# Kernel tuning notes

Measured on AMD Instinct MI355X. Metric: run time of the kernel, lower is better.

The kernel has to match this reference:

```python
import jax, jax.numpy as jnp
import numpy as np

EPS = 1e-5
NH_MHA = 8
NH_GCN = 4


def _ln(x, w, b):
    m = x.mean(-1, keepdims=True)
    v = ((x - m) ** 2).mean(-1, keepdims=True)
    return (x - m) * jax.lax.rsqrt(v + EPS) * w + b


def _mha(t, in_w, in_b, out_w, out_b):
    # torch nn.MultiheadAttention (batch_first, eval mode -> no dropout)
    B, N, C = t.shape
    hd = C // NH_MHA
    qkv = t @ in_w.T + in_b
    q, k, v = jnp.split(qkv, 3, axis=-1)
    q = q.reshape(B, N, NH_MHA, hd)
    k = k.reshape(B, N, NH_MHA, hd)
    v = v.reshape(B, N, NH_MHA, hd)
    s = jnp.einsum('bihd,bjhd->bhij', q, k) * (1.0 / np.sqrt(hd))
    a = jax.nn.softmax(s, axis=-1)
    o = jnp.einsum('bhij,bjhd->bihd', a, v).reshape(B, N, C)
    return o @ out_w.T + out_b


def _gcn(x, v_w, v_b, e1_w, e1_b, eln_w, eln_b, e2_w, e2_b, o_w, o_b, n_w, n_b):
    # GraphConvolutionNetwork.forward (query/key branches are computed but
    # unused in the original -> omitted, identical math)
    B, N, C = x.shape
    hd = C // NH_GCN
    # edge MLP: split first linear so the [B,N,N,2C] concat is never built
    w1a, w1b = e1_w[:, :C], e1_w[:, C:]
    e = (x @ w1a.T)[:, :, None, :] + (x @ w1b.T)[:, None, :, :] + e1_b  # [B,N,N,C]
    e = jax.nn.gelu(_ln(e, eln_w, eln_b), approximate=False)
    ew = e @ e2_w.T + e2_b                 # [B,Ni,Nj,H]
    adj = jax.nn.softmax(ew, axis=2)       # softmax over Nj (== dim=-1 after permute in torch)
    v = (x @ v_w.T + v_b).reshape(B, N, NH_GCN, hd)
    out = jnp.einsum('bijh,bjhd->bihd', adj, v).reshape(B, N, C)
    out = out @ o_w.T + o_b
    return _ln(out + x, n_w, n_b)          # in_features == out_features -> residual


def reference(x, mha_in_w, mha_in_b, mha_out_w, mha_out_b,
              g0_v_w, g0_v_b, g0_e1_w, g0_e1_b, g0_eln_w, g0_eln_b, g0_e2_w, g0_e2_b, g0_o_w, g0_o_b, g0_n_w, g0_n_b,
              g1_v_w, g1_v_b, g1_e1_w, g1_e1_b, g1_eln_w, g1_eln_b, g1_e2_w, g1_e2_b, g1_o_w, g1_o_b, g1_n_w, g1_n_b,
              n1_w, n1_b, n2_w, n2_b,
              f1_w, f1_b, fln_w, fln_b, f2_w, f2_b):
    B, C, H, W = x.shape
    tokens = x.reshape(B, C, H * W).transpose(0, 2, 1)  # b c h w -> b (h w) c
    attn = _mha(tokens, mha_in_w, mha_in_b, mha_out_w, mha_out_b)
    attn = _ln(attn + tokens, n1_w, n1_b)
    g = _gcn(attn, g0_v_w, g0_v_b, g0_e1_w, g0_e1_b, g0_eln_w, g0_eln_b, g0_e2_w, g0_e2_b, g0_o_w, g0_o_b, g0_n_w, g0_n_b)
    g = _gcn(g, g1_v_w, g1_v_b, g1_e1_w, g1_e1_b, g1_eln_w, g1_eln_b, g1_e2_w, g1_e2_b, g1_o_w, g1_o_b, g1_n_w, g1_n_b)
    g = _ln(g, n2_w, n2_b)
    cat = jnp.concatenate([attn, g], axis=-1)           # [B,N,2C]
    f = cat @ f1_w.T + f1_b
    f = jax.nn.gelu(_ln(f, fln_w, fln_b), approximate=False)
    f = f @ f2_w.T + f2_b
    out = tokens + f
    return out.transpose(0, 2, 1).reshape(B, C, H, W)


def setup_inputs() -> dict:
    key = jax.random.key(0)
    ks = jax.random.split(key, 8)
    B, C, H, W = 2, 128, 24, 24
    f32 = jnp.float32

    def w(k, shape):
        return jax.random.normal(k, shape, f32) * 0.02

    d = {"x": jax.random.normal(ks[0], (B, C, H, W), f32)}
    d["mha_in_w"] = w(ks[1], (3 * C, C)); d["mha_in_b"] = jnp.zeros((3 * C,), f32)
    d["mha_out_w"] = w(ks[2], (C, C)); d["mha_out_b"] = jnp.zeros((C,), f32)
    for i in range(2):
        kk = jax.random.split(ks[3 + i], 4)
        p = f"g{i}_"
        d[p + "v_w"] = w(kk[0], (C, C)); d[p + "v_b"] = jnp.zeros((C,), f32)
        d[p + "e1_w"] = w(kk[1], (C, 2 * C)); d[p + "e1_b"] = jnp.zeros((C,), f32)
        d[p + "eln_w"] = jnp.ones((C,), f32); d[p + "eln_b"] = jnp.zeros((C,), f32)
        d[p + "e2_w"] = w(kk[2], (NH_GCN, C)); d[p + "e2_b"] = jnp.zeros((NH_GCN,), f32)
        d[p + "o_w"] = w(kk[3], (C, C)); d[p + "o_b"] = jnp.zeros((C,), f32)
        d[p + "n_w"] = jnp.ones((C,), f32); d[p + "n_b"] = jnp.zeros((C,), f32)
    d["n1_w"] = jnp.ones((C,), f32); d["n1_b"] = jnp.zeros((C,), f32)
    d["n2_w"] = jnp.ones((C,), f32); d["n2_b"] = jnp.zeros((C,), f32)
    d["f1_w"] = w(ks[5], (C, 2 * C)); d["f1_b"] = jnp.zeros((C,), f32)
    d["fln_w"] = jnp.ones((C,), f32); d["fln_b"] = jnp.zeros((C,), f32)
    d["f2_w"] = w(ks[6], (C, C)); d["f2_b"] = jnp.zeros((C,), f32)
    return d
```

## Files before the change

### kernel.cpp

```cpp
#include <hip/hip_runtime.h>
#include <hip/hip_fp16.h>
#include <math.h>

#define NN 576
#define EPSV 1e-5f

typedef _Float16 h2v __attribute__((ext_vector_type(2)));
__device__ __forceinline__ float fdot2f(__half2 a, __half2 b, float c) {
    return __builtin_amdgcn_fdot2(__builtin_bit_cast(h2v, a),
                                  __builtin_bit_cast(h2v, b), c, false);
}

__device__ __forceinline__ float gelu_exact(float x) {
    return 0.5f * x * (1.0f + erff(x * 0.70710678118654752f));
}

__global__ void k_tok(const float* __restrict__ x, float* __restrict__ tok) {
    int b = blockIdx.y;
    int idx = blockIdx.x * 256 + threadIdx.x;
    if (idx < NN * 128) {
        int n = idx >> 7, c = idx & 127;
        tok[(size_t)b * NN * 128 + idx] = x[((size_t)b * 128 + c) * NN + n];
    }
}

__global__ void k_prep(const float* __restrict__ mha_in_w,
                       const float* __restrict__ e1w0, const float* __restrict__ vw0,
                       const float* __restrict__ e1w1, const float* __restrict__ vw1,
                       const float* __restrict__ lnw0, const float* __restrict__ lnb0,
                       const float* __restrict__ e2w0,
                       const float* __restrict__ lnw1, const float* __restrict__ lnb1,
                       const float* __restrict__ e2w1,
                       float* __restrict__ wTq, float* __restrict__ wT0,
                       float* __restrict__ wT1, __half* __restrict__ wh) {
    int which = blockIdx.y;
    int idx = blockIdx.x * 256 + threadIdx.x;
    if (which == 3) {
        if (idx < 1536) {
            int l = idx / 768, i2 = idx - l * 768;
            const float* lw = l ? lnw1 : lnw0;
            const float* lb = l ? lnb1 : lnb0;
            const float* e2 = l ? e2w1 : e2w0;
            float v;
            if (i2 < 128)      v = lw[i2];
            else if (i2 < 256) v = lb[i2 - 128];
            else               v = e2[i2 - 256];
            wh[idx] = __float2half(v);
        }
        return;
    }
    int k = idx / 384, o = idx - k * 384;
    if (which == 0) {
        wTq[idx] = mha_in_w[o * 128 + k];
    } else {
        const float* e1w = (which == 1) ? e1w0 : e1w1;
        const float* vw  = (which == 1) ? vw0  : vw1;
        float v;
        if (o < 128)      v = e1w[o * 256 + k];
        else if (o < 256) v = e1w[(o - 128) * 256 + 128 + k];
        else              v = vw[(o - 256) * 128 + k];
        ((which == 1) ? wT0 : wT1)[idx] = v;
    }
}

template<bool CENTER>
__global__ __launch_bounds__(384) void k_gemmT(
    const float* __restrict__ A, const float* __restrict__ wT,
    const float* __restrict__ b0, const float* __restrict__ b1, const float* __restrict__ b2,
    float* __restrict__ out)
{
    const int t = threadIdx.x;
    const int r0 = blockIdx.x * 4;
    __shared__ float a_s[4][132];
    if (t < 128) {
        float4 v = *(const float4*)(A + (size_t)(r0 + (t >> 5)) * 128 + (t & 31) * 4);
        *(float4*)&a_s[t >> 5][(t & 31) * 4] = v;
    }
    __syncthreads();
    float acc[4] = {0.f, 0.f, 0.f, 0.f};
    #pragma unroll 8
    for (int k = 0; k < 128; ++k) {
        float w = wT[(size_t)k * 384 + t];
        acc[0] += a_s[0][k] * w;
        acc[1] += a_s[1][k] * w;
        acc[2] += a_s[2][k] * w;
        acc[3] += a_s[3][k] * w;
    }
    const float* bp = (t < 128) ? b0 : ((t < 256) ? b1 : b2);
    float bv = bp ? bp[t & 127] : 0.f;
    #pragma unroll
    for (int r = 0; r < 4; ++r) acc[r] += bv;

    if (CENTER) {
        __shared__ float redc[6][4];
        const int wv = t >> 6, ln = t & 63;
        #pragma unroll
        for (int r = 0; r < 4; ++r) {
            float xr = acc[r];
            #pragma unroll
            for (int off = 32; off > 0; off >>= 1) xr += __shfl_xor(xr, off);
            if (ln == 0) redc[wv][r] = xr;
        }
        __syncthreads();
        if (t < 256) {
            const int ch = t >> 7;
            #pragma unroll
            for (int r = 0; r < 4; ++r) {
                float mean = (redc[2 * ch][r] + redc[2 * ch + 1][r]) * (1.0f / 128.0f);
                acc[r] -= mean;
            }
        }
    }
    if (t < 256) {
        #pragma unroll
        for (int r = 0; r < 4; ++r)
            ((__half*)(out + (size_t)(r0 + r) * 384))[t] = __float2half(acc[r]);
    } else {
        #pragma unroll
        for (int r = 0; r < 4; ++r)
            out[(size_t)(r0 + r) * 384 + t] = acc[r];
    }
}

__global__ __launch_bounds__(256) void k_score(
    const float* __restrict__ qkv, __half* __restrict__ sc)
{
    const int jt = blockIdx.x, it = blockIdx.y, b = blockIdx.z;
    const int i0 = it * 16, j0 = jt * 16;
    const int t = threadIdx.x;
    __shared__ __half q_s[16][136], k_s[16][136];
    for (int idx = t; idx < 512; idx += 256) {
        int tile = idx >> 8, r = (idx >> 4) & 15, cq = idx & 15;
        const __half* src = (const __half*)(qkv + (size_t)(b * NN + (tile ? j0 : i0) + r) * 384)
                            + (tile ? 128 : 0) + cq * 8;
        __half* dst = tile ? &k_s[r][cq * 8] : &q_s[r][cq * 8];
        *(uint4*)dst = *(const uint4*)src;
    }
    __syncthreads();
    const int ti = t >> 4, tj = t & 15;
    const uint4* qr = (const uint4*)q_s[ti];
    const uint4* kr = (const uint4*)k_s[tj];
    float acc[8] = {0.f,0.f,0.f,0.f,0.f,0.f,0.f,0.f};
    #pragma unroll
    for (int sstep = 0; sstep < 16; ++sstep) {
        uint4 q4 = qr[sstep], k4 = kr[sstep];
        const __half2* qh = (const __half2*)&q4;
        const __half2* kh = (const __half2*)&k4;
        #pragma unroll
        for (int p = 0; p < 4; ++p)
            acc[sstep >> 1] = fdot2f(qh[p], kh[p], acc[sstep >> 1]);
    }
    __half2 h[4];
    #pragma unroll
    for (int p = 0; p < 4; ++p)
        h[p] = __floats2half2_rn(acc[2 * p] * 0.25f, acc[2 * p + 1] * 0.25f);
    *(uint4*)(sc + ((size_t)(b * NN + i0 + ti) * NN + j0 + tj) * 8) = *(uint4*)h;
}

__global__ __launch_bounds__(256) void k_edge(
    const float* __restrict__ qkv, const __half* __restrict__ wh,
    const float* __restrict__ e2b, __half* __restrict__ ew)
{
    const int jt = blockIdx.x, it = blockIdx.y, b = blockIdx.z;
    const int i0 = it * 16, j0 = jt * 16;
    const int t = threadIdx.x;
    __shared__ __half ua_s[16][136], wb_s[16][136], wh_s[768];

    for (int idx = t; idx < 512; idx += 256) {
        int tile = idx >> 8, r = (idx >> 4) & 15, cq = idx & 15;
        const __half* src = (const __half*)(qkv + (size_t)(b * NN + (tile ? j0 : i0) + r) * 384)
                            + (tile ? 128 : 0) + cq * 8;
        __half* dst = tile ? &wb_s[r][cq * 8] : &ua_s[r][cq * 8];
        *(uint4*)dst = *(const uint4*)src;
    }
    if (t < 96) *(uint4*)&wh_s[t * 8] = *(const uint4*)&wh[t * 8];
    __syncthreads();

    const int ti = t >> 4, tj = t & 15;
    const uint4* uar = (const uint4*)ua_s[ti];
    const uint4* wbr = (const uint4*)wb_s[tj];

    float s2 = 0.f;
    #pragma unroll
    for (int sstep = 0; sstep < 16; ++sstep) {
        uint4 u4 = uar[sstep], w4 = wbr[sstep];
        const __half2* uh = (const __half2*)&u4;
        const __half2* whp = (const __half2*)&w4;
        #pragma unroll
        for (int p = 0; p < 4; ++p) {
            __half2 e = __hadd2(uh[p], whp[p]);
            s2 = fdot2f(e, e, s2);
        }
    }
    const float rstd = rsqrtf(s2 * (1.0f / 128.0f) + EPSV);
    const __half2 rh   = __float2half2_rn(rstd);
    const __half2 cexp = __float2half2_rn(-2.4554672f);
    const __half2 one2 = __float2half2_rn(1.0f);

    float p0 = 0.f, p1 = 0.f, p2 = 0.f, p3 = 0.f;
    #pragma unroll 4
    for (int sstep = 0; sstep < 16; ++sstep) {
        uint4 u4 = uar[sstep], w4 = wbr[sstep];
        uint4 lw4 = *(const uint4*)&wh_s[sstep * 8];
        uint4 lb4 = *(const uint4*)&wh_s[128 + sstep * 8];
        uint4 q04 = *(const uint4*)&wh_s[256 + sstep * 8];
        uint4 q14 = *(const uint4*)&wh_s[384 + sstep * 8];
        uint4 q24 = *(const uint4*)&wh_s[512 + sstep * 8];
        uint4 q34 = *(const uint4*)&wh_s[640 + sstep * 8];
        const __half2* uh  = (const __half2*)&u4;
        const __half2* whp = (const __half2*)&w4;
        const __half2* lwh = (const __half2*)&lw4;
        const __half2* lbh = (const __half2*)&lb4;
        const __half2* q0h = (const __half2*)&q04;
        const __half2* q1h = (const __half2*)&q14;
        const __half2* q2h = (const __half2*)&q24;
        const __half2* q3h = (const __half2*)&q34;
        #pragma unroll
        for (int p = 0; p < 4; ++p) {
            __half2 e   = __hadd2(uh[p], whp[p]);
            __half2 rlw = __hmul2(rh, lwh[p]);
            __half2 nrm = __hfma2(e, rlw, lbh[p]);
            __half2 z   = __hmul2(nrm, cexp);
            __half2 ex  = h2exp2(z);
            __half2 den = __hadd2(ex, one2);
            __half2 rr  = h2rcp(den);
            __half2 g   = __hmul2(nrm, rr);
            p0 = fdot2f(g, q0h[p], p0);
            p1 = fdot2f(g, q1h[p], p1);
            p2 = fdot2f(g, q2h[p], p2);
            p3 = fdot2f(g, q3h[p], p3);
        }
    }
    __half2 h01 = __floats2half2_rn(p0 + e2b[0], p1 + e2b[1]);
    __half2 h23 = __floats2half2_rn(p2 + e2b[2], p3 + e2b[3]);
    __half* dst = ew + ((size_t)(b * NN + i0 + ti) * NN + j0 + tj) * 4;
    *(__half2*)dst = h01;
    *(__half2*)(dst + 2) = h23;
}

template<int NH>
__global__ __launch_bounds__(256) void k_agg(
    const float* __restrict__ resid, const float* __restrict__ vbuf,
    const __half* __restrict__ sc,
    const float* __restrict__ ow, const float* __restrict__ ob,
    const float* __restrict__ nw, const float* __restrict__ nb,
    float* __restrict__ outp)
{
    constexpr int GL = 256 / NH;
    constexpr int NE = NN / GL;
    const int bi = blockIdx.x;
    const int b = bi / NN, i = bi - b * NN;
    const int t = threadIdx.x;

    __shared__ float st_m[NH], st_i[NH];
    __shared__ float aggp[8][128];
    __shared__ float agg_s[128];
    __shared__ float op[2][128];
    __shared__ float red1[4], red2[4];

    const __half* srow = sc + (size_t)(b * NN + i) * NN * NH;

    {
        const int h = t / GL, jl = t % GL;
        float sv[NE];
        #pragma unroll
        for (int k = 0; k < NE; ++k)
            sv[k] = __half2float(srow[(size_t)(jl + k * GL) * NH + h]);
        float mx = -1e30f;
        #pragma unroll
        for (int k = 0; k < NE; ++k) mx = fmaxf(mx, sv[k]);
        #pragma unroll
        for (int off = GL / 2; off > 0; off >>= 1) mx = fmaxf(mx, __shfl_xor(mx, off));
        float sm = 0.f;
        #pragma unroll
        for (int k = 0; k < NE; ++k) sm += __expf(sv[k] - mx);
        #pragma unroll
        for (int off = GL / 2; off > 0; off >>= 1) sm += __shfl_xor(sm, off);
        if (jl == 0) { st_m[h] = mx; st_i[h] = 1.0f / sm; }
    }
    __syncthreads();

    {
        const int c4 = (t & 31) * 4, jg = t >> 5;
        const int h2 = c4 >> ((NH == 8) ? 4 : 5);
        const float m2 = st_m[h2], inv2 = st_i[h2];
        float4 acc = {0.f, 0.f, 0.f, 0.f};
        const float* vb = vbuf + 256 + c4;
        #pragma unroll 4
        for (int j = jg; j < NN; j += 8) {
            float p = __expf(__half2float(srow[(size_t)j * NH + h2]) - m2);
            const float4 v4 = *(const float4*)(vb + (size_t)(b * NN + j) * 384);
            acc.x += p * v4.x; acc.y += p * v4.y; acc.z += p * v4.z; acc.w += p * v4.w;
        }
        acc.x *= inv2; acc.y *= inv2; acc.z *= inv2; acc.w *= inv2;
        *(float4*)&aggp[jg][c4] = acc;
    }
    __syncthreads();
    if (t < 128) {
        float s = 0.f;
        #pragma unroll
        for (int gq = 0; gq < 8; ++gq) s += aggp[gq][t];
        agg_s[t] = s;
    }
    __syncthreads();

    {
        const int c = t & 127, half = t >> 7;
        float o = 0.f;
        const float4* wr = (const float4*)(ow + (size_t)c * 128 + half * 64);
        const float4* ar = (const float4*)(agg_s + half * 64);
        #pragma unroll
        for (int kq = 0; kq < 16; ++kq) {
            float4 w = wr[kq], a = ar[kq];
            o += w.x * a.x + w.y * a.y + w.z * a.z + w.w * a.w;
        }
        op[half][c] = o;
    }
    __syncthreads();
    float val = 0.f;
    if (t < 128)
        val = op[0][t] + op[1][t] + ob[t] + resid[(size_t)(b * NN + i) * 128 + t];

    float s1 = val, s2 = val * val;
    #pragma unroll
    for (int off = 32; off > 0; off >>= 1) {
        s1 += __shfl_xor(s1, off);
        s2 += __shfl_xor(s2, off);
    }
    if ((t & 63) == 0) { red1[t >> 6] = s1; red2[t >> 6] = s2; }
    __syncthreads();
    float tot1 = red1[0] + red1[1] + red1[2] + red1[3];
    float tot2 = red2[0] + red2[1] + red2[2] + red2[3];
    float mean = tot1 * (1.0f / 128.0f);
    float var = tot2 * (1.0f / 128.0f) - mean * mean;
    float rstd = rsqrtf(var + EPSV);
    if (t < 128)
        outp[(size_t)(b * NN + i) * 128 + t] = (val - mean) * rstd * nw[t] + nb[t];
}

__global__ __launch_bounds__(128) void k_final(
    const float* __restrict__ tok, const float* __restrict__ attn, const float* __restrict__ g,
    const float* __restrict__ n2w, const float* __restrict__ n2b,
    const float* __restrict__ f1w, const float* __restrict__ f1b,
    const float* __restrict__ flnw, const float* __restrict__ flnb,
    const float* __restrict__ f2w, const float* __restrict__ f2b,
    float* __restrict__ out)
{
    const int bi = blockIdx.x;
    const int b = bi / NN, i = bi - b * NN;
    const int t = threadIdx.x;
    __shared__ float cat_s[256];
    __shared__ float gl_s[128];
    __shared__ float red1[2], red2[2];

    const size_t row = (size_t)(b * NN + i) * 128;
    cat_s[t] = attn[row + t];
    float gv = g[row + t];
    {
        float s1 = gv, s2 = gv * gv;
        #pragma unroll
        for (int off = 32; off > 0; off >>= 1) { s1 += __shfl_xor(s1, off); s2 += __shfl_xor(s2, off); }
        if ((t & 63) == 0) { red1[t >> 6] = s1; red2[t >> 6] = s2; }
        __syncthreads();
        float mean = (red1[0] + red1[1]) * (1.0f / 128.0f);
        float var = (red2[0] + red2[1]) * (1.0f / 128.0f) - mean * mean;
        float rstd = rsqrtf(var + EPSV);
        cat_s[128 + t] = (gv - mean) * rstd * n2w[t] + n2b[t];
    }
    __syncthreads();
    float f = f1b[t];
    {
        const float4* wr = reinterpret_cast<const float4*>(f1w + (size_t)t * 256);
        const float4* cr = reinterpret_cast<const float4*>(cat_s);
        #pragma unroll 8
        for (int kq = 0; kq < 64; ++kq) {
            float4 w = wr[kq], c = cr[kq];
            f += w.x * c.x + w.y * c.y + w.z * c.z + w.w * c.w;
        }
    }
    {
        float s1 = f, s2 = f * f;
        #pragma unroll
        for (int off = 32; off > 0; off >>= 1) { s1 += __shfl_xor(s1, off); s2 += __shfl_xor(s2, off); }
        __syncthreads();
        if ((t & 63) == 0) { red1[t >> 6] = s1; red2[t >> 6] = s2; }
        __syncthreads();
        float mean = (red1[0] + red1[1]) * (1.0f / 128.0f);
        float var = (red2[0] + red2[1]) * (1.0f / 128.0f) - mean * mean;
        float rstd = rsqrtf(var + EPSV);
        float nrm = (f - mean) * rstd * flnw[t] + flnb[t];
        gl_s[t] = gelu_exact(nrm);
    }
    __syncthreads();
    float o = f2b[t];
    {
        const float4* wr = reinterpret_cast<const float4*>(f2w + (size_t)t * 128);
        const float4* gr = reinterpret_cast<const float4*>(gl_s);
        #pragma unroll 8
        for (int kq = 0; kq < 32; ++kq) {
            float4 w = wr[kq], gg = gr[kq];
            o += w.x * gg.x + w.y * gg.y + w.z * gg.z + w.w * gg.w;
        }
    }
    out[((size_t)b * 128 + t) * NN + i] = tok[row + t] + o;
}

extern "C" void kernel_launch(void* const* d_in, const int* in_sizes, int n_in,
                              void* d_out, int out_size, void* d_ws, size_t ws_size,
                              hipStream_t stream) {
    const float* x         = (const float*)d_in[0];
    const float* mha_in_b  = (const float*)d_in[2];
    const float* mha_out_w = (const float*)d_in[3];
    const float* mha_out_b = (const float*)d_in[4];
    const float* gv_w[2]  = {(const float*)d_in[5],  (const float*)d_in[17]};
    const float* gv_b[2]  = {(const float*)d_in[6],  (const float*)d_in[18]};
    const float* ge1_w[2] = {(const float*)d_in[7],  (const float*)d_in[19]};
    const float* ge1_b[2] = {(const float*)d_in[8],  (const float*)d_in[20]};
    const float* geln_w[2]= {(const float*)d_in[9],  (const float*)d_in[21]};
    const float* geln_b[2]= {(const float*)d_in[10], (const float*)d_in[22]};
    const float* ge2_w[2] = {(const float*)d_in[11], (const float*)d_in[23]};
    const float* ge2_b[2] = {(const float*)d_in[12], (const float*)d_in[24]};
    const float* go_w[2]  = {(const float*)d_in[13], (const float*)d_in[25]};
    const float* go_b[2]  = {(const float*)d_in[14], (const float*)d_in[26]};
    const float* gn_w[2]  = {(const float*)d_in[15], (const float*)d_in[27]};
    const float* gn_b[2]  = {(const float*)d_in[16], (const float*)d_in[28]};
    const float* n1w = (const float*)d_in[29];
    const float* n1b = (const float*)d_in[30];
    const float* n2w = (const float*)d_in[31];
    const float* n2b = (const float*)d_in[32];
    const float* f1w = (const float*)d_in[33];
    const float* f1b = (const float*)d_in[34];
    const float* flnw = (const float*)d_in[35];
    const float* flnb = (const float*)d_in[36];
    const float* f2w = (const float*)d_in[37];
    const float* f2b = (const float*)d_in[38];

    float* ws     = (float*)d_ws;
    float* tokens = ws;
    float* attn   = tokens + 147456;
    float* g      = attn + 147456;
    float* qkv    = g + 147456;
    float* wTq    = qkv + 442368;
    float* wT0    = wTq + 49152;
    float* wT1    = wT0 + 49152;
    __half* wh    = (__half*)(wT1 + 49152);
    __half* sc    = wh + 2048;
    __half* ewh   = sc;

    k_tok<<<dim3(288, 2), 256, 0, stream>>>(x, tokens);
    k_prep<<<dim3(192, 4), 256, 0, stream>>>((const float*)d_in[1],
        ge1_w[0], gv_w[0], ge1_w[1], gv_w[1],
        geln_w[0], geln_b[0], ge2_w[0],
        geln_w[1], geln_b[1], ge2_w[1],
        wTq, wT0, wT1, wh);

    k_gemmT<false><<<288, 384, 0, stream>>>(tokens, wTq,
        mha_in_b, mha_in_b + 128, mha_in_b + 256, qkv);
    k_score<<<dim3(36, 36, 2), 256, 0, stream>>>(qkv, sc);
    k_agg<8><<<1152, 256, 0, stream>>>(tokens, qkv, sc, mha_out_w, mha_out_b,
                                       n1w, n1b, attn);

    for (int l = 0; l < 2; ++l) {
        const float* xin = (l == 0) ? attn : g;
        const float* wTl = (l == 0) ? wT0 : wT1;
        k_gemmT<true><<<288, 384, 0, stream>>>(xin, wTl,
            nullptr, ge1_b[l], gv_b[l], qkv);
        k_edge<<<dim3(36, 36, 2), 256, 0, stream>>>(qkv, wh + l * 768,
                                                    ge2_b[l], ewh);
        k_agg<4><<<1152, 256, 0, stream>>>(xin, qkv, ewh, go_w[l], go_b[l],
                                           gn_w[l], gn_b[l], g);
    }
    k_final<<<1152, 128, 0, stream>>>(tokens, attn, g, n2w, n2b,
        f1w, f1b, flnw, flnb, f2w, f2b, (float*)d_out);
}
```

Baseline: 229.2 us.

## Register-block edge kernel 2x2 per thread and merge setup kernels

The edge MLP kernel now computes a 2x2 block of (i,j) pairs per thread over a 32x32 tile instead of one pair over 16x16. The per-channel LayerNorm and weight values loaded from shared memory are then reused across four pairs, cutting shared-memory traffic per output. The grid shrinks to a quarter of the blocks, and register use per thread grows. The token transpose and weight-prep kernels are also merged into one launch to save a kernel launch.

```diff
diff --git a/kernel.cpp b/kernel.cpp
--- a/kernel.cpp
+++ b/kernel.cpp
@@ -15,27 +15,26 @@
     return 0.5f * x * (1.0f + erff(x * 0.70710678118654752f));
 }
 
-__global__ void k_tok(const float* __restrict__ x, float* __restrict__ tok) {
-    int b = blockIdx.y;
-    int idx = blockIdx.x * 256 + threadIdx.x;
-    if (idx < NN * 128) {
-        int n = idx >> 7, c = idx & 127;
-        tok[(size_t)b * NN * 128 + idx] = x[((size_t)b * 128 + c) * NN + n];
-    }
-}
-
-__global__ void k_prep(const float* __restrict__ mha_in_w,
-                       const float* __restrict__ e1w0, const float* __restrict__ vw0,
-                       const float* __restrict__ e1w1, const float* __restrict__ vw1,
-                       const float* __restrict__ lnw0, const float* __restrict__ lnb0,
-                       const float* __restrict__ e2w0,
-                       const float* __restrict__ lnw1, const float* __restrict__ lnb1,
-                       const float* __restrict__ e2w1,
-                       float* __restrict__ wTq, float* __restrict__ wT0,
-                       float* __restrict__ wT1, __half* __restrict__ wh) {
-    int which = blockIdx.y;
-    int idx = blockIdx.x * 256 + threadIdx.x;
-    if (which == 3) {
+__global__ void k_setup(const float* __restrict__ x, float* __restrict__ tok,
+                        const float* __restrict__ mha_in_w,
+                        const float* __restrict__ e1w0, const float* __restrict__ vw0,
+                        const float* __restrict__ e1w1, const float* __restrict__ vw1,
+                        const float* __restrict__ lnw0, const float* __restrict__ lnb0,
+                        const float* __restrict__ e2w0,
+                        const float* __restrict__ lnw1, const float* __restrict__ lnb1,
+                        const float* __restrict__ e2w1,
+                        float* __restrict__ wTq, float* __restrict__ wT0,
+                        float* __restrict__ wT1, __half* __restrict__ wh) {
+    const int which = blockIdx.y;
+    const int idx = blockIdx.x * 256 + threadIdx.x;
+    if (which < 2) {
+        if (idx < NN * 128) {
+            int n = idx >> 7, c = idx & 127;
+            tok[(size_t)which * NN * 128 + idx] = x[((size_t)which * 128 + c) * NN + n];
+        }
+        return;
+    }
+    if (which == 5) {
         if (idx < 1536) {
             int l = idx / 768, i2 = idx - l * 768;
             const float* lw = l ? lnw1 : lnw0;
@@ -49,17 +48,18 @@
         }
         return;
     }
+    if (idx >= 49152) return;
     int k = idx / 384, o = idx - k * 384;
-    if (which == 0) {
+    if (which == 2) {
         wTq[idx] = mha_in_w[o * 128 + k];
     } else {
-        const float* e1w = (which == 1) ? e1w0 : e1w1;
-        const float* vw  = (which == 1) ? vw0  : vw1;
+        const float* e1w = (which == 3) ? e1w0 : e1w1;
+        const float* vw  = (which == 3) ? vw0  : vw1;
         float v;
         if (o < 128)      v = e1w[o * 256 + k];
         else if (o < 256) v = e1w[(o - 128) * 256 + 128 + k];
         else              v = vw[(o - 256) * 128 + k];
-        ((which == 1) ? wT0 : wT1)[idx] = v;
+        ((which == 3) ? wT0 : wT1)[idx] = v;
     }
 }
 
@@ -162,12 +162,12 @@
     const float* __restrict__ e2b, __half* __restrict__ ew)
 {
     const int jt = blockIdx.x, it = blockIdx.y, b = blockIdx.z;
-    const int i0 = it * 16, j0 = jt * 16;
+    const int i0 = it * 32, j0 = jt * 32;
     const int t = threadIdx.x;
-    __shared__ __half ua_s[16][136], wb_s[16][136], wh_s[768];
-
-    for (int idx = t; idx < 512; idx += 256) {
-        int tile = idx >> 8, r = (idx >> 4) & 15, cq = idx & 15;
+    __shared__ __half ua_s[32][136], wb_s[32][136], wh_s[768];
+
+    for (int idx = t; idx < 1024; idx += 256) {
+        int tile = idx >> 9, r = (idx >> 4) & 31, cq = idx & 15;
         const __half* src = (const __half*)(qkv + (size_t)(b * NN + (tile ? j0 : i0) + r) * 384)
                             + (tile ? 128 : 0) + cq * 8;
         __half* dst = tile ? &wb_s[r][cq * 8] : &ua_s[r][cq * 8];
@@ -176,66 +176,99 @@
     if (t < 96) *(uint4*)&wh_s[t * 8] = *(const uint4*)&wh[t * 8];
     __syncthreads();
 
-    const int ti = t >> 4, tj = t & 15;
-    const uint4* uar = (const uint4*)ua_s[ti];
-    const uint4* wbr = (const uint4*)wb_s[tj];
-
-    float s2 = 0.f;
-    #pragma unroll
-    for (int sstep = 0; sstep < 16; ++sstep) {
-        uint4 u4 = uar[sstep], w4 = wbr[sstep];
-        const __half2* uh = (const __half2*)&u4;
-        const __half2* whp = (const __half2*)&w4;
+    const int ti = (t >> 4) * 2, tj = (t & 15) * 2;
+    const uint4* ua0 = (const uint4*)ua_s[ti];
+    const uint4* ua1 = (const uint4*)ua_s[ti + 1];
+    const uint4* wb0 = (const uint4*)wb_s[tj];
+    const uint4* wb1 = (const uint4*)wb_s[tj + 1];
+
+    float s2[2][2] = {{0.f, 0.f}, {0.f, 0.f}};
+    #pragma unroll 4
+    for (int ss = 0; ss < 16; ++ss) {
+        uint4 u4[2] = {ua0[ss], ua1[ss]};
+        uint4 w4[2] = {wb0[ss], wb1[ss]};
         #pragma unroll
         for (int p = 0; p < 4; ++p) {
-            __half2 e = __hadd2(uh[p], whp[p]);
-            s2 = fdot2f(e, e, s2);
-        }
-    }
-    const float rstd = rsqrtf(s2 * (1.0f / 128.0f) + EPSV);
-    const __half2 rh   = __float2half2_rn(rstd);
+            #pragma unroll
+            for (int a = 0; a < 2; ++a) {
+                const __half2 uh = ((const __half2*)&u4[a])[p];
+                #pragma unroll
+                for (int c = 0; c < 2; ++c) {
+                    __half2 e = __hadd2(uh, ((const __half2*)&w4[c])[p]);
+                    s2[a][c] = fdot2f(e, e, s2[a][c]);
+                }
+            }
+        }
+    }
+    __half2 rh[2][2];
+    #pragma unroll
+    for (int a = 0; a < 2; ++a)
+        #pragma unroll
+        for (int c = 0; c < 2; ++c)
+            rh[a][c] = __float2half2_rn(rsqrtf(s2[a][c] * (1.0f / 128.0f) + EPSV));
+
     const __half2 cexp = __float2half2_rn(-2.4554672f);
     const __half2 one2 = __float2half2_rn(1.0f);
 
-    float p0 = 0.f, p1 = 0.f, p2 = 0.f, p3 = 0.f;
-    #pragma unroll 4
-    for (int sstep = 0; sstep < 16; ++sstep) {
-        uint4 u4 = uar[sstep], w4 = wbr[sstep];
-        uint4 lw4 = *(const uint4*)&wh_s[sstep * 8];
-        uint4 lb4 = *(const uint4*)&wh_s[128 + sstep * 8];
-        uint4 q04 = *(const uint4*)&wh_s[256 + sstep * 8];
-        uint4 q14 = *(const uint4*)&wh_s[384 + sstep * 8];
-        uint4 q24 = *(const uint4*)&wh_s[512 + sstep * 8];
-        uint4 q34 = *(const uint4*)&wh_s[640 + sstep * 8];
-        const __half2* uh  = (const __half2*)&u4;
-        const __half2* whp = (const __half2*)&w4;
-        const __half2* lwh = (const __half2*)&lw4;
-        const __half2* lbh = (const __half2*)&lb4;
-        const __half2* q0h = (const __half2*)&q04;
-        const __half2* q1h = (const __half2*)&q14;
-        const __half2* q2h = (const __half2*)&q24;
-        const __half2* q3h = (const __half2*)&q34;
+    float acc[2][2][4];
+    #pragma unroll
+    for (int a = 0; a < 2; ++a)
+        #pragma unroll
+        for (int c = 0; c < 2; ++c)
+            #pragma unroll
+            for (int k = 0; k < 4; ++k) acc[a][c][k] = 0.f;
+
+    #pragma unroll 2
+    for (int ss = 0; ss < 16; ++ss) {
+        uint4 u4[2] = {ua0[ss], ua1[ss]};
+        uint4 w4[2] = {wb0[ss], wb1[ss]};
+        uint4 lw4 = *(const uint4*)&wh_s[ss * 8];
+        uint4 lb4 = *(const uint4*)&wh_s[128 + ss * 8];
+        uint4 q04 = *(const uint4*)&wh_s[256 + ss * 8];
+        uint4 q14 = *(const uint4*)&wh_s[384 + ss * 8];
+        uint4 q24 = *(const uint4*)&wh_s[512 + ss * 8];
+        uint4 q34 = *(const uint4*)&wh_s[640 + ss * 8];
         #pragma unroll
         for (int p = 0; p < 4; ++p) {
-            __half2 e   = __hadd2(uh[p], whp[p]);
-            __half2 rlw = __hmul2(rh, lwh[p]);
-            __half2 nrm = __hfma2(e, rlw, lbh[p]);
-            __half2 z   = __hmul2(nrm, cexp);
-            __half2 ex  = h2exp2(z);
-            __half2 den = __hadd2(ex, one2);
-            __half2 rr  = h2rcp(den);
-            __half2 g   = __hmul2(nrm, rr);
-            p0 = fdot2f(g, q0h[p], p0);
-            p1 = fdot2f(g, q1h[p], p1);
-            p2 = fdot2f(g, q2h[p], p2);
-            p3 = fdot2f(g, q3h[p], p3);
-        }
-    }
-    __half2 h01 = __floats2half2_rn(p0 + e2b[0], p1 + e2b[1]);
-    __half2 h23 = __floats2half2_rn(p2 + e2b[2], p3 + e2b[3]);
-    __half* dst = ew + ((size_t)(b * NN + i0 + ti) * NN + j0 + tj) * 4;
-    *(__half2*)dst = h01;
-    *(__half2*)(dst + 2) = h23;
+            const __half2 lwh = ((const __half2*)&lw4)[p];
+            const __half2 lbh = ((const __half2*)&lb4)[p];
+            const __half2 q0h = ((const __half2*)&q04)[p];
+            const __half2 q1h = ((const __half2*)&q14)[p];
+            const __half2 q2h = ((const __half2*)&q24)[p];
+            const __half2 q3h = ((const __half2*)&q34)[p];
+            #pragma unroll
+            for (int a = 0; a < 2; ++a) {
+                const __half2 uh = ((const __half2*)&u4[a])[p];
+                #pragma unroll
+                for (int c = 0; c < 2; ++c) {
+                    __half2 e   = __hadd2(uh, ((const __half2*)&w4[c])[p]);
+                    __half2 t1  = __hmul2(e, lwh);
+                    __half2 nrm = __hfma2(t1, rh[a][c], lbh);
+                    __half2 z   = __hmul2(nrm, cexp);
+                    __half2 ex  = h2exp2(z);
+                    __half2 den = __hadd2(ex, one2);
+                    __half2 rr  = h2rcp(den);
+                    __half2 g   = __hmul2(nrm, rr);
+                    acc[a][c][0] = fdot2f(g, q0h, acc[a][c][0]);
+                    acc[a][c][1] = fdot2f(g, q1h, acc[a][c][1]);
+                    acc[a][c][2] = fdot2f(g, q2h, acc[a][c][2]);
+                    acc[a][c][3] = fdot2f(g, q3h, acc[a][c][3]);
+                }
+            }
+        }
+    }
+    const float b0 = e2b[0], b1 = e2b[1], b2 = e2b[2], b3 = e2b[3];
+    #pragma unroll
+    for (int a = 0; a < 2; ++a) {
+        #pragma unroll
+        for (int c = 0; c < 2; ++c) {
+            __half2 h01 = __floats2half2_rn(acc[a][c][0] + b0, acc[a][c][1] + b1);
+            __half2 h23 = __floats2half2_rn(acc[a][c][2] + b2, acc[a][c][3] + b3);
+            __half* dst = ew + ((size_t)(b * NN + i0 + ti + a) * NN + j0 + tj + c) * 4;
+            *(__half2*)dst = h01;
+            *(__half2*)(dst + 2) = h23;
+        }
+    }
 }
 
 template<int NH>
@@ -447,8 +480,7 @@
     __half* sc    = wh + 2048;
     __half* ewh   = sc;
 
-    k_tok<<<dim3(288, 2), 256, 0, stream>>>(x, tokens);
-    k_prep<<<dim3(192, 4), 256, 0, stream>>>((const float*)d_in[1],
+    k_setup<<<dim3(288, 6), 256, 0, stream>>>(x, tokens, (const float*)d_in[1],
         ge1_w[0], gv_w[0], ge1_w[1], gv_w[1],
         geln_w[0], geln_b[0], ge2_w[0],
         geln_w[1], geln_b[1], ge2_w[1],
@@ -465,7 +497,7 @@
         const float* wTl = (l == 0) ? wT0 : wT1;
         k_gemmT<true><<<288, 384, 0, stream>>>(xin, wTl,
             nullptr, ge1_b[l], gv_b[l], qkv);
-        k_edge<<<dim3(36, 36, 2), 256, 0, stream>>>(qkv, wh + l * 768,
+        k_edge<<<dim3(18, 18, 2), 256, 0, stream>>>(qkv, wh + l * 768,
                                                     ge2_b[l], ewh);
         k_agg<4><<<1152, 256, 0, stream>>>(xin, qkv, ewh, go_w[l], go_b[l],
                                            gn_w[l], gn_b[l], g);
```

Result: no change. 232.2 us (+1.3%).
